# Kernel tuning notes

Hardware: AMD Instinct MI355X
Metric: run time of the kernel (lower is better)

The kernel has to match this reference:

```python
import jax, jax.numpy as jnp
import numpy as np

N_NODES = 50000
N_EDGES = 800000
IN_SIZE = 128
HID = 128
OUT_SIZE = 64
N_LAYERS = 2
MAXK = 32


def setup_inputs() -> dict:
    key = jax.random.key(0)
    ks = jax.random.split(key, 8)
    s = 0.05  # small init scale, xavier-like
    return {
        "x": jax.random.normal(ks[0], (N_NODES, IN_SIZE), dtype=jnp.float32),
        "W_in": jax.random.normal(ks[1], (IN_SIZE, HID), dtype=jnp.float32) * s,
        "b_in": jnp.zeros((HID,), dtype=jnp.float32),
        "W_self": jax.random.normal(ks[2], (N_LAYERS, HID, HID), dtype=jnp.float32) * s,
        "W_neigh": jax.random.normal(ks[3], (N_LAYERS, HID, HID), dtype=jnp.float32) * s,
        "W_out": jax.random.normal(ks[4], (HID, OUT_SIZE), dtype=jnp.float32) * s,
        "b_out": jnp.zeros((OUT_SIZE,), dtype=jnp.float32),
        "edge_index": jax.random.randint(ks[5], (2, N_EDGES), 0, N_NODES, dtype=jnp.int32),
        "k": MAXK,
    }


def _maxk(x, k):
    # Keep top-k values per row, zero out the rest (MaxK nonlinearity).
    vals, idx = jax.lax.top_k(x, k)                     # [N, k]
    rows = jnp.arange(x.shape[0])[:, None]
    return jnp.zeros_like(x).at[rows, idx].set(vals)


def reference(x, W_in, b_in, W_self, W_neigh, W_out, b_out, edge_index, k):
    N = x.shape[0]
    src, dst = edge_index[0], edge_index[1]
    # Row sums of the (src->dst) adjacency = out-degree of src, per original code.
    deg = jax.ops.segment_sum(jnp.ones((src.shape[0],), dtype=x.dtype), src,
                              num_segments=N)[:, None]  # [N, 1]
    h = x @ W_in + b_in                                  # lin_in
    for i in range(W_self.shape[0]):
        hs = _maxk(h, k)                                 # MaxK sparsify [N, H]
        # adj @ hs : out[i] = sum over edges (i -> j) of hs[j]; then mean-normalize
        agg = jax.ops.segment_sum(hs[dst], src, num_segments=N) / (deg + 1e-6)
        h = hs @ W_self[i] + agg @ W_neigh[i]            # h_self + h_neigh
        # dropout (eval) and Identity norm are no-ops
    return h @ W_out + b_out                             # lin_out
```

## Files before the change

kernel.cpp:

```cpp
#include <hip/hip_runtime.h>

#define KDIM 128
#define NNODE 50000
#define CHSTRIDE 800000

typedef _Float16 f16x8 __attribute__((ext_vector_type(8)));
typedef _Float16 f16x4 __attribute__((ext_vector_type(4)));
typedef float f32x16 __attribute__((ext_vector_type(16)));

#define NRANGE 6250
#define ECHUNK 3200

__global__ void hist_kernel(const int* __restrict__ src, int* __restrict__ cnt, int E) {
    const int r = blockIdx.x & 7;
    const int chunk = blockIdx.x >> 3;
    const int lo = r * NRANGE, hi = lo + NRANGE;
    const int base = chunk * ECHUNK;
    const int end = min(base + ECHUNK, E);
    for (int i = base + threadIdx.x; i < end; i += 256) {
        int s = src[i];
        if (s >= lo && s < hi) atomicAdd(&cnt[s], 1);
    }
}

__global__ void scatter_kernel(const int* __restrict__ src, const int* __restrict__ dst,
                               int* cursor, int* __restrict__ col, int E) {
    const int r = blockIdx.x & 7;
    const int chunk = blockIdx.x >> 3;
    const int lo = r * NRANGE, hi = lo + NRANGE;
    const int base = chunk * ECHUNK;
    const int end = min(base + ECHUNK, E);
    for (int i = base + threadIdx.x; i < end; i += 256) {
        int s = src[i];
        if (s >= lo && s < hi) {
            int p = atomicAdd(&cursor[s], 1);
            col[p] = dst[i];
        }
    }
}

__global__ void scan1_kernel(const int* __restrict__ cnt, int* __restrict__ row_ptr,
                             int* __restrict__ bsum, int N) {
    __shared__ int ws[4];
    const int t = threadIdx.x;
    const int lane = t & 63, w = t >> 6;
    const int i = blockIdx.x * 256 + t;
    int v = (i < N) ? cnt[i] : 0;
    int x = v;
    #pragma unroll
    for (int off = 1; off < 64; off <<= 1) {
        int u = __shfl_up(x, off);
        if (lane >= off) x += u;
    }
    if (lane == 63) ws[w] = x;
    __syncthreads();
    int wexcl = 0;
    #pragma unroll
    for (int k = 0; k < 4; k++) wexcl += (k < w) ? ws[k] : 0;
    if (i < N) row_ptr[i] = wexcl + x - v;
    if (t == 255) bsum[blockIdx.x] = wexcl + x;
}

__global__ void scan2_kernel(int* __restrict__ bsum, int NB) {
    __shared__ int ws[4];
    const int t = threadIdx.x;
    const int lane = t & 63, w = t >> 6;
    int v = (t < NB) ? bsum[t] : 0;
    int x = v;
    #pragma unroll
    for (int off = 1; off < 64; off <<= 1) {
        int u = __shfl_up(x, off);
        if (lane >= off) x += u;
    }
    if (lane == 63) ws[w] = x;
    __syncthreads();
    int wexcl = 0;
    #pragma unroll
    for (int k = 0; k < 4; k++) wexcl += (k < w) ? ws[k] : 0;
    if (t < NB) bsum[t] = wexcl + x - v;
}

__global__ void scan3_kernel(const int* __restrict__ bsum, int* __restrict__ row_ptr,
                             int* __restrict__ cursor, int N, int E) {
    const int i = blockIdx.x * 256 + threadIdx.x;
    if (i < N) {
        int v = row_ptr[i] + bsum[blockIdx.x];
        row_ptr[i] = v;
        cursor[i] = v;
    }
    if (i == 0) row_ptr[N] = E;
}

__global__ void sortrows_kernel(const int* __restrict__ row_ptr, int* __restrict__ col, int M) {
    int wid = (blockIdx.x * blockDim.x + threadIdx.x) >> 6;
    int lane = threadIdx.x & 63;
    if (wid >= M) return;
    int s = row_ptr[wid], e = row_ptr[wid + 1], len = e - s;
    if (len <= 1) return;
    if (len <= 64) {
        int v = (lane < len) ? col[s + lane] : 0x7fffffff;
        #pragma unroll
        for (int k = 2; k <= 64; k <<= 1) {
            #pragma unroll
            for (int j = k >> 1; j > 0; j >>= 1) {
                int o = __shfl_xor(v, j);
                bool dir = ((lane & k) == 0);
                bool smaller = ((lane & j) == 0);
                int mn = min(v, o), mx = max(v, o);
                v = (dir == smaller) ? mn : mx;
            }
        }
        if (lane < len) col[s + lane] = v;
    } else if (lane == 0) {
        for (int a = s + 1; a < e; a++) {
            int key = col[a];
            int b = a - 1;
            while (b >= s && col[b] > key) { col[b + 1] = col[b]; b--; }
            col[b + 1] = key;
        }
    }
}

__device__ __forceinline__ float2 maxk_row(float2 v, int lane) {
    unsigned int u0 = __float_as_uint(v.x);
    u0 = (u0 & 0x80000000u) ? ~u0 : (u0 | 0x80000000u);
    unsigned int u1 = __float_as_uint(v.y);
    u1 = (u1 & 0x80000000u) ? ~u1 : (u1 | 0x80000000u);

    unsigned int prefix = 0;
    int remaining = 32;
    #pragma unroll
    for (int b = 31; b >= 0; --b) {
        unsigned int candHi = (prefix >> b) | 1u;
        unsigned long long m0 = __ballot((u0 >> b) == candHi);
        unsigned long long m1 = __ballot((u1 >> b) == candHi);
        int cnt = __popcll(m0) + __popcll(m1);
        if (cnt >= remaining) prefix |= (1u << b);
        else remaining -= cnt;
    }

    unsigned long long e0 = __ballot(u0 == prefix);
    unsigned long long e1 = __ballot(u1 == prefix);
    unsigned long long g0 = __ballot(u0 > prefix);
    unsigned long long g1 = __ballot(u1 > prefix);
    int quota = 32 - (__popcll(g0) + __popcll(g1));
    unsigned long long below = (1ULL << lane) - 1ULL;
    int rank0 = __popcll(e0 & below) + __popcll(e1 & below);
    int rank1 = rank0 + (int)((e0 >> lane) & 1ULL);
    bool k0 = (u0 > prefix) || (((e0 >> lane) & 1ULL) && rank0 < quota);
    bool k1 = (u1 > prefix) || (((e1 >> lane) & 1ULL) && rank1 < quota);

    float2 o;
    o.x = k0 ? v.x : 0.0f;
    o.y = k1 ? v.y : 0.0f;
    return o;
}

#define ANPB 16
#define AECAP 1024

__global__ __launch_bounds__(256)
void aggregate_kernel(const float* __restrict__ hsc, const int* __restrict__ row_ptr,
                      const int* __restrict__ col, float* __restrict__ agg, int M) {
    __shared__ int cols[AECAP];
    const int c = blockIdx.x & 7;
    const int g = blockIdx.x >> 3;
    const int n0 = g * ANPB;
    const int tid = threadIdx.x;
    const int w = tid >> 6;
    const int lane = tid & 63;
    const int ng = lane >> 4;
    const int e2 = (lane >> 3) & 1;
    const int f2 = lane & 7;

    const int nend = min(n0 + ANPB, M);
    const int base0 = row_ptr[n0];
    const int ecount = row_ptr[nend] - base0;
    const bool fits = (ecount <= AECAP);
    if (fits) {
        for (int i = tid; i < ecount; i += 256) cols[i] = col[base0 + i];
    }
    __syncthreads();

    const int n = n0 + w * 4 + ng;
    const bool valid = (n < M);
    const int s = valid ? (row_ptr[n] - base0) : 0;
    const int e = valid ? (row_ptr[n + 1] - base0) : 0;
    const char* bp = (const char*)(hsc + (size_t)c * CHSTRIDE) + f2 * 8;

    float ax = 0.f, ay = 0.f, bx = 0.f, by = 0.f;
    int j = s + e2;
    if (fits) {
        for (; j + 2 < e; j += 4) {
            unsigned o0 = (unsigned)cols[j] << 6;
            unsigned o1 = (unsigned)cols[j + 2] << 6;
            float2 v0 = *(const float2*)(bp + o0);
            float2 v1 = *(const float2*)(bp + o1);
            ax += v0.x; ay += v0.y;
            bx += v1.x; by += v1.y;
        }
        if (j < e) {
            float2 v = *(const float2*)(bp + ((unsigned)cols[j] << 6));
            ax += v.x; ay += v.y;
        }
    } else {
        const int* cg = col + base0;
        for (; j + 2 < e; j += 4) {
            unsigned o0 = (unsigned)cg[j] << 6;
            unsigned o1 = (unsigned)cg[j + 2] << 6;
            float2 v0 = *(const float2*)(bp + o0);
            float2 v1 = *(const float2*)(bp + o1);
            ax += v0.x; ay += v0.y;
            bx += v1.x; by += v1.y;
        }
        if (j < e) {
            float2 v = *(const float2*)(bp + ((unsigned)cg[j] << 6));
            ax += v.x; ay += v.y;
        }
    }

    float tx = ax + bx, ty = ay + by;
    tx += __shfl_xor(tx, 8);
    ty += __shfl_xor(ty, 8);
    if (valid && e2 == 0) {
        float inv = 1.0f / ((float)(e - s) + 1e-6f);
        float2 o;
        o.x = tx * inv;
        o.y = ty * inv;
        ((float2*)(agg + (size_t)n * KDIM + c * 16))[f2] = o;
    }
}

__global__ void conv_wt_kernel(const float* __restrict__ W_in,
                               const float* __restrict__ W_self,
                               const float* __restrict__ W_neigh,
                               const float* __restrict__ W_out,
                               _Float16* __restrict__ wb) {
    int t = blockIdx.x * blockDim.x + threadIdx.x;
    if (t < 81920) {
        int m = t >> 14;
        int e = t & 16383;
        int n = e >> 7, k = e & 127;
        const float* S = (m == 0) ? W_in
                       : (m <= 2) ? (W_self + (size_t)(m - 1) * 16384)
                                  : (W_neigh + (size_t)(m - 3) * 16384);
        float v = S[k * 128 + n];
        _Float16 hi = (_Float16)v;
        _Float16 lo = (_Float16)(v - (float)hi);
        int pair = m * 2;
        wb[(size_t)pair * 16384 + n * 128 + k] = hi;
        wb[(size_t)(pair + 1) * 16384 + n * 128 + k] = lo;
    } else if (t < 90112) {
        int e = t - 81920;
        int n = e >> 7, k = e & 127;
        float v = W_out[k * 64 + n];
        _Float16 hi = (_Float16)v;
        _Float16 lo = (_Float16)(v - (float)hi);
        wb[(size_t)10 * 16384 + e] = hi;
        wb[(size_t)11 * 16384 + e] = lo;
    }
}

template <int BN, bool DUAL, bool BIAS, bool A1CHUNK, bool FUSE_MAXK>
__global__ __launch_bounds__(256)
void gemm_mfma(const float* __restrict__ A1, const float* __restrict__ A2,
               const _Float16* __restrict__ B1h, const _Float16* __restrict__ B1l,
               const _Float16* __restrict__ B2h, const _Float16* __restrict__ B2l,
               const float* __restrict__ bias, float* __restrict__ C,
               float* __restrict__ hsc_out, int M) {
    constexpr int BM = (BN == 128) ? 32 : 64;
    constexpr int NSRC = DUAL ? 2 : 1;
    constexpr int AREG = BM / 8;
    constexpr int LOOFF = BM * 256;

    __shared__ __align__(16) char Alds[2 * BM * 256];

    const int tid = threadIdx.x;
    const int w = tid >> 6;
    const int lane = tid & 63;
    const int l31 = lane & 31;
    const int kslot = lane >> 5;
    const int row0 = blockIdx.x * BM;

    const int n0 = (BN == 128) ? w * 32 : (w & 1) * 32;
    const int mt0 = (BN == 128) ? 0 : (w >> 1);

    const int srow = tid >> 5;
    const int k4 = tid & 31;

    f32x16 acc;
    #pragma unroll
    for (int e = 0; e < 16; e++) acc[e] = 0.0f;

    float4 pa[AREG];
    #pragma unroll
    for (int p = 0; p < AREG; p++) {
        int row = srow + p * 8;
        float4 v = make_float4(0.f, 0.f, 0.f, 0.f);
        if (row0 + row < M) {
            if (A1CHUNK)
                v = *(const float4*)(A1 + (size_t)(k4 >> 2) * CHSTRIDE
                                        + (size_t)(row0 + row) * 16 + (k4 & 3) * 4);
            else
                v = *(const float4*)(A1 + (size_t)(row0 + row) * KDIM + k4 * 4);
        }
        pa[p] = v;
    }

    #pragma unroll
    for (int s = 0; s < NSRC; s++) {
        if (s) __syncthreads();
        const _Float16* Bh = s ? B2h : B1h;
        const _Float16* Bl = s ? B2l : B1l;
        const _Float16* bph = Bh + (size_t)(n0 + l31) * 128 + kslot * 8;
        const _Float16* bpl = Bl + (size_t)(n0 + l31) * 128 + kslot * 8;
        f16x8 bhr[8], blr[8];
        #pragma unroll
        for (int kb = 0; kb < 8; kb++) {
            bhr[kb] = *(const f16x8*)(bph + kb * 16);
            blr[kb] = *(const f16x8*)(bpl + kb * 16);
        }

        #pragma unroll
        for (int p = 0; p < AREG; p++) {
            int row = srow + p * 8;
            float4 v = pa[p];
            _Float16 h0 = (_Float16)v.x, h1 = (_Float16)v.y,
                     h2 = (_Float16)v.z, h3 = (_Float16)v.w;
            f16x4 hv = {h0, h1, h2, h3};
            f16x4 lv = {(_Float16)(v.x - (float)h0), (_Float16)(v.y - (float)h1),
                        (_Float16)(v.z - (float)h2), (_Float16)(v.w - (float)h3)};
            int boff = (k4 * 8) ^ ((row & 7) << 4);
            *(f16x4*)(Alds + row * 256 + boff) = hv;
            *(f16x4*)(Alds + LOOFF + row * 256 + boff) = lv;
        }
        __syncthreads();

        if (s + 1 < NSRC) {
            #pragma unroll
            for (int p = 0; p < AREG; p++) {
                int row = srow + p * 8;
                float4 v = make_float4(0.f, 0.f, 0.f, 0.f);
                if (row0 + row < M)
                    v = *(const float4*)(A2 + (size_t)(row0 + row) * KDIM + k4 * 4);
                pa[p] = v;
            }
        }

        const int arow = mt0 * 32 + l31;
        #pragma unroll
        for (int kb = 0; kb < 8; kb++) {
            int boff = ((kb * 2 + kslot) * 16) ^ ((arow & 7) << 4);
            const char* rp = Alds + arow * 256 + boff;
            f16x8 ah = *(const f16x8*)(rp);
            f16x8 al = *(const f16x8*)(rp + LOOFF);
            acc = __builtin_amdgcn_mfma_f32_32x32x16_f16(al, bhr[kb], acc, 0, 0, 0);
            acc = __builtin_amdgcn_mfma_f32_32x32x16_f16(ah, blr[kb], acc, 0, 0, 0);
            acc = __builtin_amdgcn_mfma_f32_32x32x16_f16(ah, bhr[kb], acc, 0, 0, 0);
        }
    }

    float bv = 0.0f;
    if (BIAS) bv = bias[n0 + l31];

    if constexpr (FUSE_MAXK) {
        __syncthreads();
        float* ht = (float*)Alds;
        #pragma unroll
        for (int r = 0; r < 16; r++) {
            int row = (r & 3) + 8 * (r >> 2) + 4 * kslot;
            ht[row * 128 + n0 + l31] = acc[r] + bv;
        }
        __syncthreads();
        float* slab = hsc_out + (size_t)(lane >> 3) * CHSTRIDE;
        #pragma unroll 1
        for (int rr = 0; rr < BM / 4; rr++) {
            int row = w * (BM / 4) + rr;
            float2 v = *(const float2*)(ht + row * 128 + lane * 2);
            float2 o = maxk_row(v, lane);
            int n = row0 + row;
            if (n < M)
                ((float2*)slab)[(size_t)n * 8 + (lane & 7)] = o;
        }
    } else {
        #pragma unroll
        for (int r = 0; r < 16; r++) {
            int row = row0 + mt0 * 32 + (r & 3) + 8 * (r >> 2) + 4 * kslot;
            if (row < M) C[(size_t)row * BN + n0 + l31] = acc[r] + bv;
        }
    }
}

extern "C" void kernel_launch(void* const* d_in, const int* in_sizes, int n_in,
                              void* d_out, int out_size, void* d_ws, size_t ws_size,
                              hipStream_t stream) {
    const float* x       = (const float*)d_in[0];
    const float* W_in    = (const float*)d_in[1];
    const float* b_in    = (const float*)d_in[2];
    const float* W_self  = (const float*)d_in[3];
    const float* W_neigh = (const float*)d_in[4];
    const float* W_out   = (const float*)d_in[5];
    const float* b_out   = (const float*)d_in[6];
    const int*   eidx    = (const int*)d_in[7];

    const int N = NNODE, E = 800000;
    const int* src = eidx;
    const int* dst = eidx + E;

    char* ws = (char*)d_ws;
    float* slabA = (float*)(ws);
    float* slabB = (float*)(ws + 25600000);
    float* agg   = (float*)(ws + 51200000);
    int* cnt     = (int*)(ws + 76800000);
    int* row_ptr = (int*)(ws + 77000000);
    int* cursor  = (int*)(ws + 77200016);
    int* col     = (int*)(ws + 77400016);
    _Float16* wb = (_Float16*)(ws + 80600016);
    int* bsum    = (int*)(ws + 81000016);

    const _Float16* WinT_h  = wb + (size_t)0 * 16384;
    const _Float16* WinT_l  = wb + (size_t)1 * 16384;
    const _Float16* WoutT_h = wb + (size_t)10 * 16384;
    const _Float16* WoutT_l = wb + (size_t)11 * 16384;

    const int NB = (N + 255) / 256;
    const int EG = ((E + ECHUNK - 1) / ECHUNK) * 8;
    const int AG = ((N + ANPB - 1) / ANPB) * 8;
    const int G32 = (N + 31) / 32;
    const int G64 = (N + 63) / 64;

    hipMemsetAsync(cnt, 0, N * sizeof(int), stream);
    hist_kernel<<<EG, 256, 0, stream>>>(src, cnt, E);
    scan1_kernel<<<NB, 256, 0, stream>>>(cnt, row_ptr, bsum, N);
    scan2_kernel<<<1, 256, 0, stream>>>(bsum, NB);
    scan3_kernel<<<NB, 256, 0, stream>>>(bsum, row_ptr, cursor, N, E);
    scatter_kernel<<<EG, 256, 0, stream>>>(src, dst, cursor, col, E);
    sortrows_kernel<<<(N + 3) / 4, 256, 0, stream>>>(row_ptr, col, N);
    conv_wt_kernel<<<(90112 + 255) / 256, 256, 0, stream>>>(W_in, W_self, W_neigh, W_out, wb);

    gemm_mfma<128, false, true, false, true><<<G32, 256, 0, stream>>>(
        x, nullptr, WinT_h, WinT_l, nullptr, nullptr, b_in, nullptr, slabA, N);

    aggregate_kernel<<<AG, 256, 0, stream>>>(slabA, row_ptr, col, agg, N);
    gemm_mfma<128, true, false, true, true><<<G32, 256, 0, stream>>>(
        slabA, agg, wb + (size_t)2 * 16384, wb + (size_t)3 * 16384,
        wb + (size_t)6 * 16384, wb + (size_t)7 * 16384, nullptr, nullptr, slabB, N);

    aggregate_kernel<<<AG, 256, 0, stream>>>(slabB, row_ptr, col, agg, N);
    gemm_mfma<128, true, false, true, false><<<G32, 256, 0, stream>>>(
        slabB, agg, wb + (size_t)4 * 16384, wb + (size_t)5 * 16384,
        wb + (size_t)8 * 16384, wb + (size_t)9 * 16384, nullptr, slabA, nullptr, N);

    gemm_mfma<64, false, true, false, false><<<G64, 256, 0, stream>>>(
        slabA, nullptr, WoutT_h, WoutT_l, nullptr, nullptr, b_out, (float*)d_out, nullptr, N);
}
```

Baseline: 364.1 us.

## Store MaxK activations compressed as values plus byte indices for sparse aggregation

The fused MaxK epilogue now writes each row as 32 kept values plus 32 uint8 column indices, replacing the dense channel-chunked slab. Aggregation gathers only these 32 entries per neighbor and scatters them with LDS atomics into per-wave accumulators. The following GEMM scatters the compressed row back into dense shared-memory tiles. This cuts gather traffic per edge to roughly a quarter, but adds shared-memory atomic contention and removes the per-channel grid split.

```diff
diff --git a/kernel.cpp b/kernel.cpp
--- a/kernel.cpp
+++ b/kernel.cpp
@@ -2,7 +2,6 @@
 
 #define KDIM 128
 #define NNODE 50000
-#define CHSTRIDE 800000
 
 typedef _Float16 f16x8 __attribute__((ext_vector_type(8)));
 typedef _Float16 f16x4 __attribute__((ext_vector_type(4)));
@@ -121,7 +120,7 @@
     }
 }
 
-__device__ __forceinline__ float2 maxk_row(float2 v, int lane) {
+__device__ __forceinline__ float2 maxk_row(float2 v, int lane, bool& k0o, bool& k1o) {
     unsigned int u0 = __float_as_uint(v.x);
     u0 = (u0 & 0x80000000u) ? ~u0 : (u0 | 0x80000000u);
     unsigned int u1 = __float_as_uint(v.y);
@@ -150,6 +149,8 @@
     bool k0 = (u0 > prefix) || (((e0 >> lane) & 1ULL) && rank0 < quota);
     bool k1 = (u1 > prefix) || (((e1 >> lane) & 1ULL) && rank1 < quota);
 
+    k0o = k0;
+    k1o = k1;
     float2 o;
     o.x = k0 ? v.x : 0.0f;
     o.y = k1 ? v.y : 0.0f;
@@ -157,21 +158,20 @@
 }
 
 #define ANPB 16
-#define AECAP 1024
+#define AECAP 512
 
 __global__ __launch_bounds__(256)
-void aggregate_kernel(const float* __restrict__ hsc, const int* __restrict__ row_ptr,
-                      const int* __restrict__ col, float* __restrict__ agg, int M) {
+void aggregate_kernel(const float* __restrict__ cv, const unsigned char* __restrict__ ci,
+                      const int* __restrict__ row_ptr, const int* __restrict__ col,
+                      float* __restrict__ agg, int M) {
     __shared__ int cols[AECAP];
-    const int c = blockIdx.x & 7;
-    const int g = blockIdx.x >> 3;
-    const int n0 = g * ANPB;
+    __shared__ float acc[4][2][128];
+    const int n0 = blockIdx.x * ANPB;
     const int tid = threadIdx.x;
     const int w = tid >> 6;
     const int lane = tid & 63;
-    const int ng = lane >> 4;
-    const int e2 = (lane >> 3) & 1;
-    const int f2 = lane & 7;
+    const int h = lane >> 5;
+    const int l32 = lane & 31;
 
     const int nend = min(n0 + ANPB, M);
     const int base0 = row_ptr[n0];
@@ -182,52 +182,62 @@
     }
     __syncthreads();
 
-    const int n = n0 + w * 4 + ng;
-    const bool valid = (n < M);
-    const int s = valid ? (row_ptr[n] - base0) : 0;
-    const int e = valid ? (row_ptr[n + 1] - base0) : 0;
-    const char* bp = (const char*)(hsc + (size_t)c * CHSTRIDE) + f2 * 8;
-
-    float ax = 0.f, ay = 0.f, bx = 0.f, by = 0.f;
-    int j = s + e2;
-    if (fits) {
-        for (; j + 2 < e; j += 4) {
-            unsigned o0 = (unsigned)cols[j] << 6;
-            unsigned o1 = (unsigned)cols[j + 2] << 6;
-            float2 v0 = *(const float2*)(bp + o0);
-            float2 v1 = *(const float2*)(bp + o1);
-            ax += v0.x; ay += v0.y;
-            bx += v1.x; by += v1.y;
-        }
-        if (j < e) {
-            float2 v = *(const float2*)(bp + ((unsigned)cols[j] << 6));
-            ax += v.x; ay += v.y;
-        }
-    } else {
-        const int* cg = col + base0;
-        for (; j + 2 < e; j += 4) {
-            unsigned o0 = (unsigned)cg[j] << 6;
-            unsigned o1 = (unsigned)cg[j + 2] << 6;
-            float2 v0 = *(const float2*)(bp + o0);
-            float2 v1 = *(const float2*)(bp + o1);
-            ax += v0.x; ay += v0.y;
-            bx += v1.x; by += v1.y;
-        }
-        if (j < e) {
-            float2 v = *(const float2*)(bp + ((unsigned)cg[j] << 6));
-            ax += v.x; ay += v.y;
-        }
-    }
-
-    float tx = ax + bx, ty = ay + by;
-    tx += __shfl_xor(tx, 8);
-    ty += __shfl_xor(ty, 8);
-    if (valid && e2 == 0) {
+    float* aw = &acc[w][0][0];
+    float* ah = &acc[w][h][0];
+
+    #pragma unroll 1
+    for (int u = 0; u < 4; u++) {
+        int n = n0 + w * 4 + u;
+        if (n >= M) break;
+        #pragma unroll
+        for (int q = 0; q < 4; q++) aw[lane + q * 64] = 0.0f;
+
+        int s = row_ptr[n] - base0, e = row_ptr[n + 1] - base0;
+        int j = s + h;
+        if (fits) {
+            for (; j + 6 < e; j += 8) {
+                int c0 = cols[j];     int c1 = cols[j + 2];
+                int c2 = cols[j + 4]; int c3 = cols[j + 6];
+                float v0 = cv[(size_t)c0 * 32 + l32]; int i0 = ci[(size_t)c0 * 32 + l32];
+                float v1 = cv[(size_t)c1 * 32 + l32]; int i1 = ci[(size_t)c1 * 32 + l32];
+                float v2 = cv[(size_t)c2 * 32 + l32]; int i2 = ci[(size_t)c2 * 32 + l32];
+                float v3 = cv[(size_t)c3 * 32 + l32]; int i3 = ci[(size_t)c3 * 32 + l32];
+                atomicAdd(&ah[i0], v0);
+                atomicAdd(&ah[i1], v1);
+                atomicAdd(&ah[i2], v2);
+                atomicAdd(&ah[i3], v3);
+            }
+            for (; j < e; j += 2) {
+                int c0 = cols[j];
+                float v0 = cv[(size_t)c0 * 32 + l32]; int i0 = ci[(size_t)c0 * 32 + l32];
+                atomicAdd(&ah[i0], v0);
+            }
+        } else {
+            const int* cg = col + base0;
+            for (; j + 6 < e; j += 8) {
+                int c0 = cg[j];     int c1 = cg[j + 2];
+                int c2 = cg[j + 4]; int c3 = cg[j + 6];
+                float v0 = cv[(size_t)c0 * 32 + l32]; int i0 = ci[(size_t)c0 * 32 + l32];
+                float v1 = cv[(size_t)c1 * 32 + l32]; int i1 = ci[(size_t)c1 * 32 + l32];
+                float v2 = cv[(size_t)c2 * 32 + l32]; int i2 = ci[(size_t)c2 * 32 + l32];
+                float v3 = cv[(size_t)c3 * 32 + l32]; int i3 = ci[(size_t)c3 * 32 + l32];
+                atomicAdd(&ah[i0], v0);
+                atomicAdd(&ah[i1], v1);
+                atomicAdd(&ah[i2], v2);
+                atomicAdd(&ah[i3], v3);
+            }
+            for (; j < e; j += 2) {
+                int c0 = cg[j];
+                float v0 = cv[(size_t)c0 * 32 + l32]; int i0 = ci[(size_t)c0 * 32 + l32];
+                atomicAdd(&ah[i0], v0);
+            }
+        }
+
         float inv = 1.0f / ((float)(e - s) + 1e-6f);
-        float2 o;
-        o.x = tx * inv;
-        o.y = ty * inv;
-        ((float2*)(agg + (size_t)n * KDIM + c * 16))[f2] = o;
+        float r0 = (acc[w][0][lane]      + acc[w][1][lane])      * inv;
+        float r1 = (acc[w][0][lane + 64] + acc[w][1][lane + 64]) * inv;
+        agg[(size_t)n * KDIM + lane]      = r0;
+        agg[(size_t)n * KDIM + lane + 64] = r1;
     }
 }
 
@@ -261,13 +271,15 @@
     }
 }
 
-template <int BN, bool DUAL, bool BIAS, bool A1CHUNK, bool FUSE_MAXK>
+template <int BN, bool DUAL, bool BIAS, bool A1COMP, bool FUSE_MAXK>
 __global__ __launch_bounds__(256)
-void gemm_mfma(const float* __restrict__ A1, const float* __restrict__ A2,
+void gemm_mfma(const float* __restrict__ A1,
+               const float* __restrict__ cv1, const unsigned char* __restrict__ ci1,
+               const float* __restrict__ A2,
                const _Float16* __restrict__ B1h, const _Float16* __restrict__ B1l,
                const _Float16* __restrict__ B2h, const _Float16* __restrict__ B2l,
                const float* __restrict__ bias, float* __restrict__ C,
-               float* __restrict__ hsc_out, int M) {
+               float* __restrict__ cv_out, unsigned char* __restrict__ ci_out, int M) {
     constexpr int BM = (BN == 128) ? 32 : 64;
     constexpr int NSRC = DUAL ? 2 : 1;
     constexpr int AREG = BM / 8;
@@ -285,26 +297,33 @@
     const int n0 = (BN == 128) ? w * 32 : (w & 1) * 32;
     const int mt0 = (BN == 128) ? 0 : (w >> 1);
 
-    const int srow = tid >> 5;
+    const int srow32 = tid >> 5;
     const int k4 = tid & 31;
+    const int crow = tid >> 3;
+    const int cg = tid & 7;
 
     f32x16 acc;
     #pragma unroll
     for (int e = 0; e < 16; e++) acc[e] = 0.0f;
 
     float4 pa[AREG];
-    #pragma unroll
-    for (int p = 0; p < AREG; p++) {
-        int row = srow + p * 8;
-        float4 v = make_float4(0.f, 0.f, 0.f, 0.f);
-        if (row0 + row < M) {
-            if (A1CHUNK)
-                v = *(const float4*)(A1 + (size_t)(k4 >> 2) * CHSTRIDE
-                                        + (size_t)(row0 + row) * 16 + (k4 & 3) * 4);
-            else
+    float4 pv = make_float4(0.f, 0.f, 0.f, 0.f);
+    unsigned int pid = 0;
+
+    if constexpr (A1COMP) {
+        if (row0 + crow < M) {
+            pv = *(const float4*)(cv1 + (size_t)(row0 + crow) * 32 + cg * 4);
+            pid = *(const unsigned int*)(ci1 + (size_t)(row0 + crow) * 32 + cg * 4);
+        }
+    } else {
+        #pragma unroll
+        for (int p = 0; p < AREG; p++) {
+            int row = srow32 + p * 8;
+            float4 v = make_float4(0.f, 0.f, 0.f, 0.f);
+            if (row0 + row < M)
                 v = *(const float4*)(A1 + (size_t)(row0 + row) * KDIM + k4 * 4);
-        }
-        pa[p] = v;
+            pa[p] = v;
+        }
     }
 
     #pragma unroll
@@ -321,25 +340,47 @@
             blr[kb] = *(const f16x8*)(bpl + kb * 16);
         }
 
-        #pragma unroll
-        for (int p = 0; p < AREG; p++) {
-            int row = srow + p * 8;
-            float4 v = pa[p];
-            _Float16 h0 = (_Float16)v.x, h1 = (_Float16)v.y,
-                     h2 = (_Float16)v.z, h3 = (_Float16)v.w;
-            f16x4 hv = {h0, h1, h2, h3};
-            f16x4 lv = {(_Float16)(v.x - (float)h0), (_Float16)(v.y - (float)h1),
-                        (_Float16)(v.z - (float)h2), (_Float16)(v.w - (float)h3)};
-            int boff = (k4 * 8) ^ ((row & 7) << 4);
-            *(f16x4*)(Alds + row * 256 + boff) = hv;
-            *(f16x4*)(Alds + LOOFF + row * 256 + boff) = lv;
+        if (A1COMP && s == 0) {
+            #pragma unroll
+            for (int q = 0; q < 2; q++) {
+                float4 z = make_float4(0.f, 0.f, 0.f, 0.f);
+                *(float4*)(Alds + crow * 256 + cg * 32 + q * 16) = z;
+                *(float4*)(Alds + LOOFF + crow * 256 + cg * 32 + q * 16) = z;
+            }
+            if (row0 + crow < M) {
+                #pragma unroll
+                for (int e2 = 0; e2 < 4; e2++) {
+                    float val = (e2 == 0) ? pv.x : (e2 == 1) ? pv.y
+                              : (e2 == 2) ? pv.z : pv.w;
+                    int f = (pid >> (8 * e2)) & 255;
+                    _Float16 hi = (_Float16)val;
+                    _Float16 lo = (_Float16)(val - (float)hi);
+                    int boff = (((f >> 3) * 16) ^ ((crow & 7) << 4)) + ((f & 7) * 2);
+                    *(_Float16*)(Alds + crow * 256 + boff) = hi;
+                    *(_Float16*)(Alds + LOOFF + crow * 256 + boff) = lo;
+                }
+            }
+        } else {
+            #pragma unroll
+            for (int p = 0; p < AREG; p++) {
+                int row = srow32 + p * 8;
+                float4 v = pa[p];
+                _Float16 h0 = (_Float16)v.x, h1 = (_Float16)v.y,
+                         h2 = (_Float16)v.z, h3 = (_Float16)v.w;
+                f16x4 hv = {h0, h1, h2, h3};
+                f16x4 lv = {(_Float16)(v.x - (float)h0), (_Float16)(v.y - (float)h1),
+                            (_Float16)(v.z - (float)h2), (_Float16)(v.w - (float)h3)};
+                int boff = (k4 * 8) ^ ((row & 7) << 4);
+                *(f16x4*)(Alds + row * 256 + boff) = hv;
+                *(f16x4*)(Alds + LOOFF + row * 256 + boff) = lv;
+            }
         }
         __syncthreads();
 
         if (s + 1 < NSRC) {
             #pragma unroll
             for (int p = 0; p < AREG; p++) {
-                int row = srow + p * 8;
+                int row = srow32 + p * 8;
                 float4 v = make_float4(0.f, 0.f, 0.f, 0.f);
                 if (row0 + row < M)
                     v = *(const float4*)(A2 + (size_t)(row0 + row) * KDIM + k4 * 4);
@@ -372,15 +413,28 @@
             ht[row * 128 + n0 + l31] = acc[r] + bv;
         }
         __syncthreads();
-        float* slab = hsc_out + (size_t)(lane >> 3) * CHSTRIDE;
+        const unsigned long long below = (1ULL << lane) - 1ULL;
         #pragma unroll 1
         for (int rr = 0; rr < BM / 4; rr++) {
             int row = w * (BM / 4) + rr;
             float2 v = *(const float2*)(ht + row * 128 + lane * 2);
-            float2 o = maxk_row(v, lane);
+            bool k0, k1;
+            maxk_row(v, lane, k0, k1);
+            unsigned long long km0 = __ballot(k0);
+            unsigned long long km1 = __ballot(k1);
+            int c0 = __popcll(km0 & below) + __popcll(km1 & below);
+            int c1 = c0 + (k0 ? 1 : 0);
             int n = row0 + row;
-            if (n < M)
-                ((float2*)slab)[(size_t)n * 8 + (lane & 7)] = o;
+            if (n < M) {
+                if (k0) {
+                    cv_out[(size_t)n * 32 + c0] = v.x;
+                    ci_out[(size_t)n * 32 + c0] = (unsigned char)(2 * lane);
+                }
+                if (k1) {
+                    cv_out[(size_t)n * 32 + c1] = v.y;
+                    ci_out[(size_t)n * 32 + c1] = (unsigned char)(2 * lane + 1);
+                }
+            }
         }
     } else {
         #pragma unroll
@@ -408,8 +462,11 @@
     const int* dst = eidx + E;
 
     char* ws = (char*)d_ws;
-    float* slabA = (float*)(ws);
-    float* slabB = (float*)(ws + 25600000);
+    float* h3            = (float*)(ws);
+    float* cvA           = (float*)(ws + 25600000);
+    unsigned char* ciA   = (unsigned char*)(ws + 32000000);
+    float* cvB           = (float*)(ws + 33600000);
+    unsigned char* ciB   = (unsigned char*)(ws + 40000000);
     float* agg   = (float*)(ws + 51200000);
     int* cnt     = (int*)(ws + 76800000);
     int* row_ptr = (int*)(ws + 77000000);
@@ -425,7 +482,7 @@
 
     const int NB = (N + 255) / 256;
     const int EG = ((E + ECHUNK - 1) / ECHUNK) * 8;
-    const int AG = ((N + ANPB - 1) / ANPB) * 8;
+    const int AG = (N + ANPB - 1) / ANPB;
     const int G32 = (N + 31) / 32;
     const int G64 = (N + 63) / 64;
 
@@ -439,18 +496,20 @@
     conv_wt_kernel<<<(90112 + 255) / 256, 256, 0, stream>>>(W_in, W_self, W_neigh, W_out, wb);
 
     gemm_mfma<128, false, true, false, true><<<G32, 256, 0, stream>>>(
-        x, nullptr, WinT_h, WinT_l, nullptr, nullptr, b_in, nullptr, slabA, N);
-
-    aggregate_kernel<<<AG, 256, 0, stream>>>(slabA, row_ptr, col, agg, N);
+        x, nullptr, nullptr, nullptr, WinT_h, WinT_l, nullptr, nullptr,
+        b_in, nullptr, cvA, ciA, N);
+
+    aggregate_kernel<<<AG, 256, 0, stream>>>(cvA, ciA, row_ptr, col, agg, N);
     gemm_mfma<128, true, false, true, true><<<G32, 256, 0, stream>>>(
-        slabA, agg, wb + (size_t)2 * 16384, wb + (size_t)3 * 16384,
-        wb + (size_t)6 * 16384, wb + (size_t)7 * 16384, nullptr, nullptr, slabB, N);
-
-    aggregate_kernel<<<AG, 256, 0, stream>>>(slabB, row_ptr, col, agg, N);
+        nullptr, cvA, ciA, agg, wb + (size_t)2 * 16384, wb + (size_t)3 * 16384,
+        wb + (size_t)6 * 16384, wb + (size_t)7 * 16384, nullptr, nullptr, cvB, ciB, N);
+
+    aggregate_kernel<<<AG, 256, 0, stream>>>(cvB, ciB, row_ptr, col, agg, N);
     gemm_mfma<128, true, false, true, false><<<G32, 256, 0, stream>>>(
-        slabB, agg, wb + (size_t)4 * 16384, wb + (size_t)5 * 16384,
-        wb + (size_t)8 * 16384, wb + (size_t)9 * 16384, nullptr, slabA, nullptr, N);
+        nullptr, cvB, ciB, agg, wb + (size_t)4 * 16384, wb + (size_t)5 * 16384,
+        wb + (size_t)8 * 16384, wb + (size_t)9 * 16384, nullptr, h3, nullptr, nullptr, N);
 
     gemm_mfma<64, false, true, false, false><<<G64, 256, 0, stream>>>(
-        slabA, nullptr, WoutT_h, WoutT_l, nullptr, nullptr, b_out, (float*)d_out, nullptr, N);
-}
+        h3, nullptr, nullptr, nullptr, WoutT_h, WoutT_l, nullptr, nullptr,
+        b_out, (float*)d_out, nullptr, nullptr, N);
+}
```

Result: slower. 543.3 us (+49.2%).
